# Optimization experiments

Measured on AMD Instinct MI355X. Metric: run time of the kernel, lower is better.

Reference implementation:

```python
import jax, jax.numpy as jnp
import numpy as np
import math

N_HEADS = 16
EMBED = 1024
D_KEY = EMBED // N_HEADS
B, S = 2, 2048
NEG = -1000000000.0


def setup_inputs() -> dict:
    key = jax.random.key(0)
    ks = jax.random.split(key, 7)
    scale = 1.0 / math.sqrt(EMBED)
    x = jax.random.normal(ks[0], (B, S, EMBED), dtype=jnp.float32)
    Wq_w = jax.random.uniform(ks[1], (EMBED, EMBED), jnp.float32, -scale, scale)
    Wq_b = jax.random.uniform(ks[2], (EMBED,), jnp.float32, -scale, scale)
    Wk_w = jax.random.uniform(ks[3], (EMBED, EMBED), jnp.float32, -scale, scale)
    Wk_b = jax.random.uniform(ks[4], (EMBED,), jnp.float32, -scale, scale)
    Wv_w = jax.random.uniform(ks[5], (EMBED, EMBED), jnp.float32, -scale, scale)
    Wv_b = jax.random.uniform(ks[6], (EMBED,), jnp.float32, -scale, scale)
    return {"x": x, "Wq_w": Wq_w, "Wq_b": Wq_b, "Wk_w": Wk_w, "Wk_b": Wk_b,
            "Wv_w": Wv_w, "Wv_b": Wv_b, "is_masked": 1}


def reference(x, Wq_w, Wq_b, Wk_w, Wk_b, Wv_w, Wv_b, is_masked):
    b, s, e = x.shape
    # nn.Linear: y = x @ W.T + b
    q = x @ Wq_w.T + Wq_b
    k = x @ Wk_w.T + Wk_b
    v = x @ Wv_w.T + Wv_b
    # [B, H, S, Dk]
    q = q.reshape(b, s, N_HEADS, D_KEY).transpose(0, 2, 1, 3)
    k = k.reshape(b, s, N_HEADS, D_KEY).transpose(0, 2, 1, 3)
    v = v.reshape(b, s, N_HEADS, D_KEY).transpose(0, 2, 1, 3)
    scores = jnp.einsum("bhqd,bhkd->bhqk", q, k) / math.sqrt(D_KEY)
    # non-standard mask: keep positions where score != padding (0)
    mask = scores != 0.0
    if is_masked:
        causal = jnp.tril(jnp.ones((1, s, s), dtype=bool))  # broadcasts over B,H
        mask = causal[None] & mask  # [1,1,S,S] & [B,H,S,S]
    scores = jnp.where(mask, scores, NEG)
    probs = jax.nn.softmax(scores, axis=-1)
    out = jnp.einsum("bhqk,bhkd->bhqd", probs, v)
    return out.transpose(0, 2, 1, 3).reshape(b, s, e)
```

## Files before the change

kernel.cpp:

```cpp
#include <hip/hip_runtime.h>

#define B_SZ   2
#define NH     16
#define S_LEN  2048
#define DK     64
#define EMB    1024
#define M_TOT  (B_SZ * S_LEN)
#define KT     64

typedef float          f32x4  __attribute__((ext_vector_type(4)));
typedef float          f32x16 __attribute__((ext_vector_type(16)));
typedef unsigned int   u32x4  __attribute__((ext_vector_type(4)));
typedef unsigned short u16x8  __attribute__((ext_vector_type(8)));
typedef unsigned short u16x4  __attribute__((ext_vector_type(4)));
typedef __bf16         bf16x8 __attribute__((ext_vector_type(8)));

static __device__ __forceinline__ f32x4 mfma16(u16x8 a, u16x8 b, f32x4 c) {
    return __builtin_amdgcn_mfma_f32_16x16x32_bf16(
        __builtin_bit_cast(bf16x8, a), __builtin_bit_cast(bf16x8, b), c, 0, 0, 0);
}
static __device__ __forceinline__ f32x16 mfma32(u16x8 a, u16x8 b, f32x16 c) {
    return __builtin_amdgcn_mfma_f32_32x32x16_bf16(
        __builtin_bit_cast(bf16x8, a), __builtin_bit_cast(bf16x8, b), c, 0, 0, 0);
}

static __device__ __forceinline__ unsigned short f2bf(float f) {
    unsigned int u = __builtin_bit_cast(unsigned int, f);
    u = (u + 0x7FFFu + ((u >> 16) & 1u)) >> 16;
    return (unsigned short)u;
}

static __device__ __forceinline__ float exp2_hw(float x) {
    float r; asm("v_exp_f32 %0, %1" : "=v"(r) : "v"(x)); return r;
}

#define GLDS16(g, l)  __builtin_amdgcn_global_load_lds(                      \
    (const void __attribute__((address_space(1)))*)(g),                      \
    (void __attribute__((address_space(3)))*)(l), 16, 0, 0)

__global__ __launch_bounds__(256) void cvt_kernel(
    const float* __restrict__ x,  const float* __restrict__ wq,
    const float* __restrict__ wk, const float* __restrict__ wv,
    unsigned short* __restrict__ xb,  unsigned short* __restrict__ wqb,
    unsigned short* __restrict__ wkb, unsigned short* __restrict__ wvb)
{
    long gid = (long)blockIdx.x * 256 + threadIdx.x;
    long e = gid * 4;
    const float* src; unsigned short* dst; long off;
    if      (e < 4194304L) { src = x;  dst = xb;  off = e; }
    else if (e < 5242880L) { src = wq; dst = wqb; off = e - 4194304L; }
    else if (e < 6291456L) { src = wk; dst = wkb; off = e - 5242880L; }
    else                   { src = wv; dst = wvb; off = e - 6291456L; }
    f32x4 v = *(const f32x4*)(src + off);
    u16x4 u;
    u[0] = f2bf(v[0]); u[1] = f2bf(v[1]); u[2] = f2bf(v[2]); u[3] = f2bf(v[3]);
    *(u16x4*)(dst + off) = u;
}

#define BM 128
#define BN 128
#define BK 64

__global__ __launch_bounds__(256) void qkv_gemm(
    const unsigned short* __restrict__ xb,
    const unsigned short* __restrict__ wb,
    const float* __restrict__ bq, const float* __restrict__ bk,
    const float* __restrict__ bv,
    unsigned short* __restrict__ qkv)
{
    const int tid  = threadIdx.x;
    const int lane = tid & 63;
    const int wid  = tid >> 6;
    const int wm   = wid >> 1, wn = wid & 1;
    const int n0   = blockIdx.x * BN;
    const int m0   = blockIdx.y * BM;
    const int mat  = blockIdx.z;

    const unsigned short* wmat = wb + (size_t)mat * (1024 * 1024);
    const float* bias = (mat == 0) ? bq : ((mat == 1) ? bk : bv);
    unsigned short* dst = qkv + (size_t)mat * ((size_t)M_TOT * EMB);

    __shared__ __align__(16) unsigned short Al[BM * 64];
    __shared__ __align__(16) unsigned short Bl[BN * 64];

    f32x4 acc[4][4];
#pragma unroll
    for (int i = 0; i < 4; ++i)
#pragma unroll
        for (int j = 0; j < 4; ++j)
            acc[i][j] = (f32x4){0.f, 0.f, 0.f, 0.f};

    const int wrow = wid * 32;
    const int lrow = lane >> 3;
    const int lcol = ((lane & 7) ^ lrow) * 8;
    const int l15  = lane & 15;
    const int sl0 = (((lane >> 4))     ^ (l15 & 7)) * 8;
    const int sl1 = ((4 + (lane >> 4)) ^ (l15 & 7)) * 8;

    for (int k0 = 0; k0 < EMB; k0 += BK) {
        const unsigned short* ga = xb   + (size_t)(m0 + wrow + lrow) * EMB + k0 + lcol;
        const unsigned short* gb = wmat + (size_t)(n0 + wrow + lrow) * EMB + k0 + lcol;
#pragma unroll
        for (int j = 0; j < 4; ++j) {
            GLDS16(ga + (size_t)j * 8 * EMB, &Al[(wrow + j * 8) * 64]);
            GLDS16(gb + (size_t)j * 8 * EMB, &Bl[(wrow + j * 8) * 64]);
        }
        __syncthreads();

#pragma unroll
        for (int kk = 0; kk < 2; ++kk) {
            const int sl = kk ? sl1 : sl0;
            u16x8 a[4], b[4];
#pragma unroll
            for (int i = 0; i < 4; ++i)
                a[i] = *(const u16x8*)&Al[(wm * 64 + i * 16 + l15) * 64 + sl];
#pragma unroll
            for (int j = 0; j < 4; ++j)
                b[j] = *(const u16x8*)&Bl[(wn * 64 + j * 16 + l15) * 64 + sl];
#pragma unroll
            for (int i = 0; i < 4; ++i)
#pragma unroll
                for (int j = 0; j < 4; ++j)
                    acc[i][j] = mfma16(a[i], b[j], acc[i][j]);
        }
        __syncthreads();
    }

#pragma unroll
    for (int j = 0; j < 4; ++j) {
        int n = n0 + wn * 64 + j * 16 + l15;
        float bvv = bias[n];
        int h = n >> 6, d = n & 63;
#pragma unroll
        for (int i = 0; i < 4; ++i) {
#pragma unroll
            for (int r = 0; r < 4; ++r) {
                int m = m0 + wm * 64 + i * 16 + ((lane >> 4) << 2) + r;
                int bb = m >> 11, s = m & 2047;
                dst[((size_t)((bb * NH + h) * S_LEN + s)) * DK + d] =
                    f2bf(acc[i][j][r] + bvv);
            }
        }
    }
}

__global__ __launch_bounds__(512) void attn_kernel(
    const unsigned short* __restrict__ Q,
    const unsigned short* __restrict__ K,
    const unsigned short* __restrict__ V,
    const int* __restrict__ mskp,
    float* __restrict__ out)
{
    const int tid = threadIdx.x, lane = tid & 63, wid = tid >> 6;
    const int grp = wid >> 2, qw = wid & 3;
    const int l31 = lane & 31, H = lane >> 5;
    const int bh = blockIdx.x;
    const int h  = bh & 15, b = bh >> 4;
    const int y  = blockIdx.y;
    const int qt = (y < 8) ? y : 23 - y;
    const int q0 = qt * 128;
    const size_t hoff = ((size_t)(b * NH + h)) * S_LEN * DK;
    const unsigned short* Qh = Q + hoff;
    const unsigned short* Kh = K + hoff;
    const unsigned short* Vh = V + hoff;
    const int msk = *mskp;
    const int ntiles = msk ? (2 * qt + 2) : (S_LEN / KT);
    const int niter  = ntiles >> 1;

    __shared__ __align__(16) unsigned short Kl[2][2][64 * 64];
    __shared__ __align__(16) unsigned short Vt[2][2][64 * 64];
    __shared__ float MLbuf[512];

    const int qrow = q0 + qw * 32 + l31;
    u16x8 qf[4];
#pragma unroll
    for (int ks = 0; ks < 4; ++ks)
        qf[ks] = *(const u16x8*)(Qh + (size_t)qrow * DK + ks * 16 + H * 8);

    u16x8 ones1;
#pragma unroll
    for (int i = 0; i < 8; ++i) ones1[i] = 0x3F80;

    f32x16 o0, o1, lacc;
#pragma unroll
    for (int i = 0; i < 16; ++i) { o0[i] = 0.f; o1[i] = 0.f; lacc[i] = 0.f; }
    float mx = -1e30f;

    const int gt  = tid & 255;
    const int sr0 = gt >> 3, sc8 = gt & 7, sr1 = sr0 + 32;
    const int kwo0 = sr0 * 64 + ((sc8 ^ (sr0 & 7)) << 3);
    const int kwo1 = sr1 * 64 + ((sc8 ^ (sr1 & 7)) << 3);
    const int vwo0 = (((sr0 >> 3) ^ sc8) << 3) + (sr0 & 7);
    const int vwo1 = (((sr1 >> 3) ^ sc8) << 3) + (sr1 & 7);

    const int qmin = q0 + qw * 32;
    const int dsw0 = l31 >> 3, dsw1 = 4 + (l31 >> 3);
    const int rsw  = l31 & 7;
    const float SC2 = 0.125f * 1.4426950408889634f;

    u16x8 kr[2], vr[2];
    {
        const unsigned short* K0 = Kh + (size_t)grp * KT * DK;
        const unsigned short* V0 = Vh + (size_t)grp * KT * DK;
        kr[0] = *(const u16x8*)(K0 + (size_t)sr0 * DK + sc8 * 8);
        vr[0] = *(const u16x8*)(V0 + (size_t)sr0 * DK + sc8 * 8);
        kr[1] = *(const u16x8*)(K0 + (size_t)sr1 * DK + sc8 * 8);
        vr[1] = *(const u16x8*)(V0 + (size_t)sr1 * DK + sc8 * 8);
        unsigned short* Kg = Kl[grp][0];
        unsigned short* Vg = Vt[grp][0];
        *(u16x8*)&Kg[kwo0] = kr[0];
        *(u16x8*)&Kg[kwo1] = kr[1];
#pragma unroll
        for (int e = 0; e < 8; ++e) {
            Vg[(sc8 * 8 + e) * 64 + vwo0] = vr[0][e];
            Vg[(sc8 * 8 + e) * 64 + vwo1] = vr[1][e];
        }
        if (grp + 2 < ntiles) {
            const unsigned short* Kn = Kh + (size_t)(grp + 2) * KT * DK;
            const unsigned short* Vn = Vh + (size_t)(grp + 2) * KT * DK;
            kr[0] = *(const u16x8*)(Kn + (size_t)sr0 * DK + sc8 * 8);
            vr[0] = *(const u16x8*)(Vn + (size_t)sr0 * DK + sc8 * 8);
            kr[1] = *(const u16x8*)(Kn + (size_t)sr1 * DK + sc8 * 8);
            vr[1] = *(const u16x8*)(Vn + (size_t)sr1 * DK + sc8 * 8);
        }
    }
    __syncthreads();

    int cur = 0;
    for (int it = 0; it < niter; ++it) {
        const int kt = 2 * it + grp;

        if (kt + 2 < ntiles) {
            unsigned short* Kg = Kl[grp][cur ^ 1];
            unsigned short* Vg = Vt[grp][cur ^ 1];
            *(u16x8*)&Kg[kwo0] = kr[0];
            *(u16x8*)&Kg[kwo1] = kr[1];
#pragma unroll
            for (int e = 0; e < 8; ++e) {
                Vg[(sc8 * 8 + e) * 64 + vwo0] = vr[0][e];
                Vg[(sc8 * 8 + e) * 64 + vwo1] = vr[1][e];
            }
        }
        if (kt + 4 < ntiles) {
            const unsigned short* Kn = Kh + (size_t)(kt + 4) * KT * DK;
            const unsigned short* Vn = Vh + (size_t)(kt + 4) * KT * DK;
            kr[0] = *(const u16x8*)(Kn + (size_t)sr0 * DK + sc8 * 8);
            vr[0] = *(const u16x8*)(Vn + (size_t)sr0 * DK + sc8 * 8);
            kr[1] = *(const u16x8*)(Kn + (size_t)sr1 * DK + sc8 * 8);
            vr[1] = *(const u16x8*)(Vn + (size_t)sr1 * DK + sc8 * 8);
        }

        if (!(msk && kt * KT > qmin + 31)) {
            const unsigned short* Kg = Kl[grp][cur];
            const unsigned short* Vg = Vt[grp][cur];

            f32x16 st0, st1;
#pragma unroll
            for (int i = 0; i < 16; ++i) { st0[i] = 0.f; st1[i] = 0.f; }
            __builtin_amdgcn_s_setprio(1);
#pragma unroll
            for (int ks = 0; ks < 4; ++ks) {
                const int g = (((ks << 1) + H) ^ rsw) << 3;
                u16x8 kf0 = *(const u16x8*)&Kg[l31 * 64 + g];
                u16x8 kf1 = *(const u16x8*)&Kg[(32 + l31) * 64 + g];
                st0 = mfma32(kf0, qf[ks], st0);
                st1 = mfma32(kf1, qf[ks], st1);
            }
            __builtin_amdgcn_s_setprio(0);

            st0 *= SC2;
            st1 *= SC2;
            float p[32];
#pragma unroll
            for (int r = 0; r < 16; ++r) { p[r] = st0[r]; p[16 + r] = st1[r]; }
            const bool needmask = msk && (kt * KT + 63 > qrow);
            if (needmask) {
#pragma unroll
                for (int r = 0; r < 16; ++r) {
                    const int krow = (r & 3) + 8 * (r >> 2) + 4 * H;
                    if (kt * KT + krow > qrow)      p[r]      = -1e30f;
                    if (kt * KT + 32 + krow > qrow) p[16 + r] = -1e30f;
                }
            }

            float t8[8];
#pragma unroll
            for (int i = 0; i < 8; ++i)
                t8[i] = fmaxf(fmaxf(p[i], p[i + 8]), fmaxf(p[i + 16], p[i + 24]));
#pragma unroll
            for (int i = 0; i < 4; ++i) t8[i] = fmaxf(t8[i], t8[i + 4]);
            float mt = fmaxf(fmaxf(t8[0], t8[1]), fmaxf(t8[2], t8[3]));
            mt = fmaxf(mt, __shfl_xor(mt, 32, 64));

            if (!__all(mt <= mx + 11.54f)) {
                const float mn = fmaxf(mx, mt);
                const float al = exp2_hw(mx - mn);
                mx = mn;
                o0 *= al; o1 *= al;
                lacc[0] *= al;
            }

#pragma unroll
            for (int r = 0; r < 32; ++r) p[r] = exp2_hw(p[r] - mx);

            __builtin_amdgcn_s_setprio(1);
#pragma unroll
            for (int ks = 0; ks < 4; ++ks) {
                const int bb = ks * 8;
                unsigned int wa, wb2, wc, wd;
                asm("v_cvt_pk_bf16_f32 %0, %1, %2" : "=v"(wa)  : "v"(p[bb + 0]), "v"(p[bb + 1]));
                asm("v_cvt_pk_bf16_f32 %0, %1, %2" : "=v"(wb2) : "v"(p[bb + 2]), "v"(p[bb + 3]));
                asm("v_cvt_pk_bf16_f32 %0, %1, %2" : "=v"(wc)  : "v"(p[bb + 4]), "v"(p[bb + 5]));
                asm("v_cvt_pk_bf16_f32 %0, %1, %2" : "=v"(wd)  : "v"(p[bb + 6]), "v"(p[bb + 7]));
                asm volatile("v_permlane32_swap_b32 %0, %1" : "+v"(wa),  "+v"(wc));
                asm volatile("v_permlane32_swap_b32 %0, %1" : "+v"(wb2), "+v"(wd));
                u32x4 wv; wv[0] = wa; wv[1] = wb2; wv[2] = wc; wv[3] = wd;
                const u16x8 pb = __builtin_bit_cast(u16x8, wv);
                const int kg = (ks << 1) + H;
                u16x8 vf0 = *(const u16x8*)&Vg[l31 * 64        + ((kg ^ dsw0) << 3)];
                u16x8 vf1 = *(const u16x8*)&Vg[(32 + l31) * 64 + ((kg ^ dsw1) << 3)];
                o0 = mfma32(vf0, pb, o0);
                o1 = mfma32(vf1, pb, o1);
                lacc = mfma32(ones1, pb, lacc);
            }
            __builtin_amdgcn_s_setprio(0);
        }

        __syncthreads();
        cur ^= 1;
    }

    const int idx = qw * 64 + lane;
    float* MO = (float*)Kl + idx * 32;
    const float lsum = lacc[0];
    if (grp == 1) {
#pragma unroll
        for (int i = 0; i < 16; ++i) {
            MO[(i + idx) & 31]      = o0[i];
            MO[(16 + i + idx) & 31] = o1[i];
        }
        MLbuf[idx * 2]     = mx;
        MLbuf[idx * 2 + 1] = lsum;
    }
    __syncthreads();
    if (grp == 0) {
        const float m2 = MLbuf[idx * 2], l2 = MLbuf[idx * 2 + 1];
        const float mn = fmaxf(mx, m2);
        const float ea = exp2_hw(mx - mn);
        const float eb = exp2_hw(m2 - mn);
        const float inv = 1.f / (lsum * ea + l2 * eb);
        float* orow = out + ((size_t)(b * S_LEN) + qrow) * EMB + h * DK;
#pragma unroll
        for (int g = 0; g < 4; ++g) {
            f32x4 w0, w1;
#pragma unroll
            for (int i = 0; i < 4; ++i) {
                w0[i] = (o0[4 * g + i] * ea + MO[(4 * g + i + idx) & 31] * eb) * inv;
                w1[i] = (o1[4 * g + i] * ea + MO[(16 + 4 * g + i + idx) & 31] * eb) * inv;
            }
            *(f32x4*)&orow[8 * g + 4 * H]      = w0;
            *(f32x4*)&orow[32 + 8 * g + 4 * H] = w1;
        }
    }
}

extern "C" void kernel_launch(void* const* d_in, const int* in_sizes, int n_in,
                              void* d_out, int out_size, void* d_ws, size_t ws_size,
                              hipStream_t stream)
{
    const float* x  = (const float*)d_in[0];
    const float* wq = (const float*)d_in[1];
    const float* bq = (const float*)d_in[2];
    const float* wk = (const float*)d_in[3];
    const float* bk = (const float*)d_in[4];
    const float* wv = (const float*)d_in[5];
    const float* bv = (const float*)d_in[6];
    const int* msk  = (const int*)d_in[7];
    float* out = (float*)d_out;

    unsigned short* xb  = (unsigned short*)d_ws;
    unsigned short* wb  = xb + (size_t)M_TOT * EMB;
    unsigned short* qkv = wb + (size_t)3 * 1024 * 1024;

    cvt_kernel<<<7168, 256, 0, stream>>>(x, wq, wk, wv,
                                         xb, wb, wb + 1024 * 1024, wb + 2 * 1024 * 1024);
    qkv_gemm<<<dim3(8, 32, 3), 256, 0, stream>>>(xb, wb, bq, bk, bv, qkv);
    attn_kernel<<<dim3(32, 16, 1), 512, 0, stream>>>(
        qkv, qkv + (size_t)M_TOT * EMB, qkv + (size_t)2 * M_TOT * EMB, msk, out);
}
```

Measured before the change: 91.77 us.

## Split KV across four wave groups and pair causal query tiles per block

The attention kernel now launches 1024-thread blocks with four KV-splitting wave groups instead of two. Each block handles two query tiles (qt and 15-qt) in sequence so causal work is balanced per block, and the grid is halved. Double buffering is dropped in favour of single-buffered shared tiles per group with two barriers per iteration. Partial results are merged through a two-level shared-memory reduction. This raises KV parallelism and balances the causal triangle, at the cost of extra synchronisation, lost load/compute overlap, and fewer blocks in flight.

```diff
diff --git a/kernel.cpp b/kernel.cpp
--- a/kernel.cpp
+++ b/kernel.cpp
@@ -144,7 +144,7 @@
     }
 }
 
-__global__ __launch_bounds__(512) void attn_kernel(
+__global__ __launch_bounds__(1024, 4) void attn_kernel(
     const unsigned short* __restrict__ Q,
     const unsigned short* __restrict__ K,
     const unsigned short* __restrict__ V,
@@ -156,35 +156,22 @@
     const int l31 = lane & 31, H = lane >> 5;
     const int bh = blockIdx.x;
     const int h  = bh & 15, b = bh >> 4;
-    const int y  = blockIdx.y;
-    const int qt = (y < 8) ? y : 23 - y;
-    const int q0 = qt * 128;
+    const int yp = blockIdx.y;
     const size_t hoff = ((size_t)(b * NH + h)) * S_LEN * DK;
     const unsigned short* Qh = Q + hoff;
     const unsigned short* Kh = K + hoff;
     const unsigned short* Vh = V + hoff;
     const int msk = *mskp;
-    const int ntiles = msk ? (2 * qt + 2) : (S_LEN / KT);
-    const int niter  = ntiles >> 1;
-
-    __shared__ __align__(16) unsigned short Kl[2][2][64 * 64];
-    __shared__ __align__(16) unsigned short Vt[2][2][64 * 64];
-    __shared__ float MLbuf[512];
-
-    const int qrow = q0 + qw * 32 + l31;
-    u16x8 qf[4];
-#pragma unroll
-    for (int ks = 0; ks < 4; ++ks)
-        qf[ks] = *(const u16x8*)(Qh + (size_t)qrow * DK + ks * 16 + H * 8);
+
+    __shared__ __align__(16) unsigned short Kl[4][64 * 64];
+    __shared__ __align__(16) unsigned short Vt[4][64 * 64];
+    __shared__ float MLbuf[3 * 512];
+    unsigned short* Kg = Kl[grp];
+    unsigned short* Vg = Vt[grp];
 
     u16x8 ones1;
 #pragma unroll
     for (int i = 0; i < 8; ++i) ones1[i] = 0x3F80;
-
-    f32x16 o0, o1, lacc;
-#pragma unroll
-    for (int i = 0; i < 16; ++i) { o0[i] = 0.f; o1[i] = 0.f; lacc[i] = 0.f; }
-    float mx = -1e30f;
 
     const int gt  = tid & 255;
     const int sr0 = gt >> 3, sc8 = gt & 7, sr1 = sr0 + 32;
@@ -193,21 +180,39 @@
     const int vwo0 = (((sr0 >> 3) ^ sc8) << 3) + (sr0 & 7);
     const int vwo1 = (((sr1 >> 3) ^ sc8) << 3) + (sr1 & 7);
 
-    const int qmin = q0 + qw * 32;
     const int dsw0 = l31 >> 3, dsw1 = 4 + (l31 >> 3);
     const int rsw  = l31 & 7;
     const float SC2 = 0.125f * 1.4426950408889634f;
-
-    u16x8 kr[2], vr[2];
-    {
-        const unsigned short* K0 = Kh + (size_t)grp * KT * DK;
-        const unsigned short* V0 = Vh + (size_t)grp * KT * DK;
-        kr[0] = *(const u16x8*)(K0 + (size_t)sr0 * DK + sc8 * 8);
-        vr[0] = *(const u16x8*)(V0 + (size_t)sr0 * DK + sc8 * 8);
-        kr[1] = *(const u16x8*)(K0 + (size_t)sr1 * DK + sc8 * 8);
-        vr[1] = *(const u16x8*)(V0 + (size_t)sr1 * DK + sc8 * 8);
-        unsigned short* Kg = Kl[grp][0];
-        unsigned short* Vg = Vt[grp][0];
+    const int idx  = qw * 64 + lane;
+
+    for (int seg = 0; seg < 2; ++seg) {
+        const int qt = seg ? (15 - yp) : yp;
+        const int q0 = qt * 128;
+        const int ntiles = msk ? (2 * qt + 2) : (S_LEN / KT);
+        const int niter  = (ntiles + 3) >> 2;
+        const int qrow = q0 + qw * 32 + l31;
+        const int qmin = q0 + qw * 32;
+
+        u16x8 qf[4];
+#pragma unroll
+        for (int ks = 0; ks < 4; ++ks)
+            qf[ks] = *(const u16x8*)(Qh + (size_t)qrow * DK + ks * 16 + H * 8);
+
+        f32x16 o0, o1, lacc;
+#pragma unroll
+        for (int i = 0; i < 16; ++i) { o0[i] = 0.f; o1[i] = 0.f; lacc[i] = 0.f; }
+        float mx = -1e30f;
+
+        u16x8 kr[2], vr[2];
+        {
+            const unsigned short* K0 = Kh + (size_t)grp * KT * DK;
+            const unsigned short* V0 = Vh + (size_t)grp * KT * DK;
+            kr[0] = *(const u16x8*)(K0 + (size_t)sr0 * DK + sc8 * 8);
+            vr[0] = *(const u16x8*)(V0 + (size_t)sr0 * DK + sc8 * 8);
+            kr[1] = *(const u16x8*)(K0 + (size_t)sr1 * DK + sc8 * 8);
+            vr[1] = *(const u16x8*)(V0 + (size_t)sr1 * DK + sc8 * 8);
+        }
+        __syncthreads();
         *(u16x8*)&Kg[kwo0] = kr[0];
         *(u16x8*)&Kg[kwo1] = kr[1];
 #pragma unroll
@@ -215,151 +220,176 @@
             Vg[(sc8 * 8 + e) * 64 + vwo0] = vr[0][e];
             Vg[(sc8 * 8 + e) * 64 + vwo1] = vr[1][e];
         }
-        if (grp + 2 < ntiles) {
-            const unsigned short* Kn = Kh + (size_t)(grp + 2) * KT * DK;
-            const unsigned short* Vn = Vh + (size_t)(grp + 2) * KT * DK;
+        if (grp + 4 < ntiles) {
+            const unsigned short* Kn = Kh + (size_t)(grp + 4) * KT * DK;
+            const unsigned short* Vn = Vh + (size_t)(grp + 4) * KT * DK;
             kr[0] = *(const u16x8*)(Kn + (size_t)sr0 * DK + sc8 * 8);
             vr[0] = *(const u16x8*)(Vn + (size_t)sr0 * DK + sc8 * 8);
             kr[1] = *(const u16x8*)(Kn + (size_t)sr1 * DK + sc8 * 8);
             vr[1] = *(const u16x8*)(Vn + (size_t)sr1 * DK + sc8 * 8);
         }
-    }
-    __syncthreads();
-
-    int cur = 0;
-    for (int it = 0; it < niter; ++it) {
-        const int kt = 2 * it + grp;
-
-        if (kt + 2 < ntiles) {
-            unsigned short* Kg = Kl[grp][cur ^ 1];
-            unsigned short* Vg = Vt[grp][cur ^ 1];
-            *(u16x8*)&Kg[kwo0] = kr[0];
-            *(u16x8*)&Kg[kwo1] = kr[1];
-#pragma unroll
-            for (int e = 0; e < 8; ++e) {
-                Vg[(sc8 * 8 + e) * 64 + vwo0] = vr[0][e];
-                Vg[(sc8 * 8 + e) * 64 + vwo1] = vr[1][e];
-            }
-        }
-        if (kt + 4 < ntiles) {
-            const unsigned short* Kn = Kh + (size_t)(kt + 4) * KT * DK;
-            const unsigned short* Vn = Vh + (size_t)(kt + 4) * KT * DK;
-            kr[0] = *(const u16x8*)(Kn + (size_t)sr0 * DK + sc8 * 8);
-            vr[0] = *(const u16x8*)(Vn + (size_t)sr0 * DK + sc8 * 8);
-            kr[1] = *(const u16x8*)(Kn + (size_t)sr1 * DK + sc8 * 8);
-            vr[1] = *(const u16x8*)(Vn + (size_t)sr1 * DK + sc8 * 8);
-        }
-
-        if (!(msk && kt * KT > qmin + 31)) {
-            const unsigned short* Kg = Kl[grp][cur];
-            const unsigned short* Vg = Vt[grp][cur];
-
-            f32x16 st0, st1;
-#pragma unroll
-            for (int i = 0; i < 16; ++i) { st0[i] = 0.f; st1[i] = 0.f; }
-            __builtin_amdgcn_s_setprio(1);
-#pragma unroll
-            for (int ks = 0; ks < 4; ++ks) {
-                const int g = (((ks << 1) + H) ^ rsw) << 3;
-                u16x8 kf0 = *(const u16x8*)&Kg[l31 * 64 + g];
-                u16x8 kf1 = *(const u16x8*)&Kg[(32 + l31) * 64 + g];
-                st0 = mfma32(kf0, qf[ks], st0);
-                st1 = mfma32(kf1, qf[ks], st1);
-            }
-            __builtin_amdgcn_s_setprio(0);
-
-            st0 *= SC2;
-            st1 *= SC2;
-            float p[32];
-#pragma unroll
-            for (int r = 0; r < 16; ++r) { p[r] = st0[r]; p[16 + r] = st1[r]; }
-            const bool needmask = msk && (kt * KT + 63 > qrow);
-            if (needmask) {
-#pragma unroll
-                for (int r = 0; r < 16; ++r) {
-                    const int krow = (r & 3) + 8 * (r >> 2) + 4 * H;
-                    if (kt * KT + krow > qrow)      p[r]      = -1e30f;
-                    if (kt * KT + 32 + krow > qrow) p[16 + r] = -1e30f;
-                }
-            }
-
-            float t8[8];
-#pragma unroll
-            for (int i = 0; i < 8; ++i)
-                t8[i] = fmaxf(fmaxf(p[i], p[i + 8]), fmaxf(p[i + 16], p[i + 24]));
-#pragma unroll
-            for (int i = 0; i < 4; ++i) t8[i] = fmaxf(t8[i], t8[i + 4]);
-            float mt = fmaxf(fmaxf(t8[0], t8[1]), fmaxf(t8[2], t8[3]));
-            mt = fmaxf(mt, __shfl_xor(mt, 32, 64));
-
-            if (!__all(mt <= mx + 11.54f)) {
-                const float mn = fmaxf(mx, mt);
-                const float al = exp2_hw(mx - mn);
-                mx = mn;
-                o0 *= al; o1 *= al;
-                lacc[0] *= al;
-            }
-
-#pragma unroll
-            for (int r = 0; r < 32; ++r) p[r] = exp2_hw(p[r] - mx);
-
-            __builtin_amdgcn_s_setprio(1);
-#pragma unroll
-            for (int ks = 0; ks < 4; ++ks) {
-                const int bb = ks * 8;
-                unsigned int wa, wb2, wc, wd;
-                asm("v_cvt_pk_bf16_f32 %0, %1, %2" : "=v"(wa)  : "v"(p[bb + 0]), "v"(p[bb + 1]));
-                asm("v_cvt_pk_bf16_f32 %0, %1, %2" : "=v"(wb2) : "v"(p[bb + 2]), "v"(p[bb + 3]));
-                asm("v_cvt_pk_bf16_f32 %0, %1, %2" : "=v"(wc)  : "v"(p[bb + 4]), "v"(p[bb + 5]));
-                asm("v_cvt_pk_bf16_f32 %0, %1, %2" : "=v"(wd)  : "v"(p[bb + 6]), "v"(p[bb + 7]));
-                asm volatile("v_permlane32_swap_b32 %0, %1" : "+v"(wa),  "+v"(wc));
-                asm volatile("v_permlane32_swap_b32 %0, %1" : "+v"(wb2), "+v"(wd));
-                u32x4 wv; wv[0] = wa; wv[1] = wb2; wv[2] = wc; wv[3] = wd;
-                const u16x8 pb = __builtin_bit_cast(u16x8, wv);
-                const int kg = (ks << 1) + H;
-                u16x8 vf0 = *(const u16x8*)&Vg[l31 * 64        + ((kg ^ dsw0) << 3)];
-                u16x8 vf1 = *(const u16x8*)&Vg[(32 + l31) * 64 + ((kg ^ dsw1) << 3)];
-                o0 = mfma32(vf0, pb, o0);
-                o1 = mfma32(vf1, pb, o1);
-                lacc = mfma32(ones1, pb, lacc);
-            }
-            __builtin_amdgcn_s_setprio(0);
-        }
-
-        __syncthreads();
-        cur ^= 1;
-    }
-
-    const int idx = qw * 64 + lane;
-    float* MO = (float*)Kl + idx * 32;
-    const float lsum = lacc[0];
-    if (grp == 1) {
-#pragma unroll
-        for (int i = 0; i < 16; ++i) {
-            MO[(i + idx) & 31]      = o0[i];
-            MO[(16 + i + idx) & 31] = o1[i];
-        }
-        MLbuf[idx * 2]     = mx;
-        MLbuf[idx * 2 + 1] = lsum;
-    }
-    __syncthreads();
-    if (grp == 0) {
-        const float m2 = MLbuf[idx * 2], l2 = MLbuf[idx * 2 + 1];
-        const float mn = fmaxf(mx, m2);
-        const float ea = exp2_hw(mx - mn);
-        const float eb = exp2_hw(m2 - mn);
-        const float inv = 1.f / (lsum * ea + l2 * eb);
-        float* orow = out + ((size_t)(b * S_LEN) + qrow) * EMB + h * DK;
-#pragma unroll
-        for (int g = 0; g < 4; ++g) {
-            f32x4 w0, w1;
-#pragma unroll
-            for (int i = 0; i < 4; ++i) {
-                w0[i] = (o0[4 * g + i] * ea + MO[(4 * g + i + idx) & 31] * eb) * inv;
-                w1[i] = (o1[4 * g + i] * ea + MO[(16 + 4 * g + i + idx) & 31] * eb) * inv;
-            }
-            *(f32x4*)&orow[8 * g + 4 * H]      = w0;
-            *(f32x4*)&orow[32 + 8 * g + 4 * H] = w1;
+        __syncthreads();
+
+        for (int it = 0; it < niter; ++it) {
+            const int kt = 4 * it + grp;
+
+            if (kt < ntiles && !(msk && kt * KT > qmin + 31)) {
+                f32x16 st0, st1;
+#pragma unroll
+                for (int i = 0; i < 16; ++i) { st0[i] = 0.f; st1[i] = 0.f; }
+                __builtin_amdgcn_s_setprio(1);
+#pragma unroll
+                for (int ks = 0; ks < 4; ++ks) {
+                    const int g = (((ks << 1) + H) ^ rsw) << 3;
+                    u16x8 kf0 = *(const u16x8*)&Kg[l31 * 64 + g];
+                    u16x8 kf1 = *(const u16x8*)&Kg[(32 + l31) * 64 + g];
+                    st0 = mfma32(kf0, qf[ks], st0);
+                    st1 = mfma32(kf1, qf[ks], st1);
+                }
+                __builtin_amdgcn_s_setprio(0);
+
+                st0 *= SC2;
+                st1 *= SC2;
+                float p[32];
+#pragma unroll
+                for (int r = 0; r < 16; ++r) { p[r] = st0[r]; p[16 + r] = st1[r]; }
+                const bool needmask = msk && (kt * KT + 63 > qrow);
+                if (needmask) {
+#pragma unroll
+                    for (int r = 0; r < 16; ++r) {
+                        const int krow = (r & 3) + 8 * (r >> 2) + 4 * H;
+                        if (kt * KT + krow > qrow)      p[r]      = -1e30f;
+                        if (kt * KT + 32 + krow > qrow) p[16 + r] = -1e30f;
+                    }
+                }
+
+                float t8[8];
+#pragma unroll
+                for (int i = 0; i < 8; ++i)
+                    t8[i] = fmaxf(fmaxf(p[i], p[i + 8]), fmaxf(p[i + 16], p[i + 24]));
+#pragma unroll
+                for (int i = 0; i < 4; ++i) t8[i] = fmaxf(t8[i], t8[i + 4]);
+                float mt = fmaxf(fmaxf(t8[0], t8[1]), fmaxf(t8[2], t8[3]));
+                mt = fmaxf(mt, __shfl_xor(mt, 32, 64));
+
+                if (!__all(mt <= mx + 11.54f)) {
+                    const float mn = fmaxf(mx, mt);
+                    const float al = exp2_hw(mx - mn);
+                    mx = mn;
+                    o0 *= al; o1 *= al;
+                    lacc[0] *= al;
+                }
+
+#pragma unroll
+                for (int r = 0; r < 32; ++r) p[r] = exp2_hw(p[r] - mx);
+
+                __builtin_amdgcn_s_setprio(1);
+#pragma unroll
+                for (int ks = 0; ks < 4; ++ks) {
+                    const int bb = ks * 8;
+                    unsigned int wa, wb2, wc, wd;
+                    asm("v_cvt_pk_bf16_f32 %0, %1, %2" : "=v"(wa)  : "v"(p[bb + 0]), "v"(p[bb + 1]));
+                    asm("v_cvt_pk_bf16_f32 %0, %1, %2" : "=v"(wb2) : "v"(p[bb + 2]), "v"(p[bb + 3]));
+                    asm("v_cvt_pk_bf16_f32 %0, %1, %2" : "=v"(wc)  : "v"(p[bb + 4]), "v"(p[bb + 5]));
+                    asm("v_cvt_pk_bf16_f32 %0, %1, %2" : "=v"(wd)  : "v"(p[bb + 6]), "v"(p[bb + 7]));
+                    asm volatile("v_permlane32_swap_b32 %0, %1" : "+v"(wa),  "+v"(wc));
+                    asm volatile("v_permlane32_swap_b32 %0, %1" : "+v"(wb2), "+v"(wd));
+                    u32x4 wv; wv[0] = wa; wv[1] = wb2; wv[2] = wc; wv[3] = wd;
+                    const u16x8 pb = __builtin_bit_cast(u16x8, wv);
+                    const int kg = (ks << 1) + H;
+                    u16x8 vf0 = *(const u16x8*)&Vg[l31 * 64        + ((kg ^ dsw0) << 3)];
+                    u16x8 vf1 = *(const u16x8*)&Vg[(32 + l31) * 64 + ((kg ^ dsw1) << 3)];
+                    o0 = mfma32(vf0, pb, o0);
+                    o1 = mfma32(vf1, pb, o1);
+                    lacc = mfma32(ones1, pb, lacc);
+                }
+                __builtin_amdgcn_s_setprio(0);
+            }
+
+            __syncthreads();
+            if (it + 1 < niter) {
+                const int ktn = 4 * (it + 1) + grp;
+                if (ktn < ntiles) {
+                    *(u16x8*)&Kg[kwo0] = kr[0];
+                    *(u16x8*)&Kg[kwo1] = kr[1];
+#pragma unroll
+                    for (int e = 0; e < 8; ++e) {
+                        Vg[(sc8 * 8 + e) * 64 + vwo0] = vr[0][e];
+                        Vg[(sc8 * 8 + e) * 64 + vwo1] = vr[1][e];
+                    }
+                }
+                if (ktn + 4 < ntiles) {
+                    const unsigned short* Kn = Kh + (size_t)(ktn + 4) * KT * DK;
+                    const unsigned short* Vn = Vh + (size_t)(ktn + 4) * KT * DK;
+                    kr[0] = *(const u16x8*)(Kn + (size_t)sr0 * DK + sc8 * 8);
+                    vr[0] = *(const u16x8*)(Vn + (size_t)sr0 * DK + sc8 * 8);
+                    kr[1] = *(const u16x8*)(Kn + (size_t)sr1 * DK + sc8 * 8);
+                    vr[1] = *(const u16x8*)(Vn + (size_t)sr1 * DK + sc8 * 8);
+                }
+                __syncthreads();
+            }
+        }
+
+        float lsum = lacc[0];
+        __syncthreads();
+        if (grp == 1 || grp == 3) {
+            float* MO = ((grp == 1) ? (float*)Kl : (float*)Vt) + idx * 32;
+#pragma unroll
+            for (int i = 0; i < 16; ++i) {
+                MO[(i + idx) & 31]      = o0[i];
+                MO[(16 + i + idx) & 31] = o1[i];
+            }
+            float* ML = MLbuf + (grp == 1 ? 0 : 512);
+            ML[idx * 2]     = mx;
+            ML[idx * 2 + 1] = lsum;
+        }
+        __syncthreads();
+        if (grp == 0 || grp == 2) {
+            const float* MO = ((grp == 0) ? (float*)Kl : (float*)Vt) + idx * 32;
+            const float* ML = MLbuf + (grp == 0 ? 0 : 512);
+            const float m2 = ML[idx * 2], l2 = ML[idx * 2 + 1];
+            const float mn = fmaxf(mx, m2);
+            const float ea = exp2_hw(mx - mn);
+            const float eb = exp2_hw(m2 - mn);
+            mx = mn;
+            lsum = lsum * ea + l2 * eb;
+#pragma unroll
+            for (int i = 0; i < 16; ++i) {
+                o0[i] = o0[i] * ea + MO[(i + idx) & 31] * eb;
+                o1[i] = o1[i] * ea + MO[(16 + i + idx) & 31] * eb;
+            }
+        }
+        __syncthreads();
+        if (grp == 2) {
+            float* MO = (float*)Kl + idx * 32;
+#pragma unroll
+            for (int i = 0; i < 16; ++i) {
+                MO[(i + idx) & 31]      = o0[i];
+                MO[(16 + i + idx) & 31] = o1[i];
+            }
+            MLbuf[1024 + idx * 2]     = mx;
+            MLbuf[1024 + idx * 2 + 1] = lsum;
+        }
+        __syncthreads();
+        if (grp == 0) {
+            const float* MO = (float*)Kl + idx * 32;
+            const float m2 = MLbuf[1024 + idx * 2], l2 = MLbuf[1024 + idx * 2 + 1];
+            const float mn = fmaxf(mx, m2);
+            const float ea = exp2_hw(mx - mn);
+            const float eb = exp2_hw(m2 - mn);
+            const float inv = 1.f / (lsum * ea + l2 * eb);
+            float* orow = out + ((size_t)(b * S_LEN) + qrow) * EMB + h * DK;
+#pragma unroll
+            for (int g = 0; g < 4; ++g) {
+                f32x4 w0, w1;
+#pragma unroll
+                for (int i = 0; i < 4; ++i) {
+                    w0[i] = (o0[4 * g + i] * ea + MO[(4 * g + i + idx) & 31] * eb) * inv;
+                    w1[i] = (o1[4 * g + i] * ea + MO[(16 + 4 * g + i + idx) & 31] * eb) * inv;
+                }
+                *(f32x4*)&orow[8 * g + 4 * H]      = w0;
+                *(f32x4*)&orow[32 + 8 * g + 4 * H] = w1;
+            }
         }
     }
 }
@@ -385,6 +415,6 @@
     cvt_kernel<<<7168, 256, 0, stream>>>(x, wq, wk, wv,
                                          xb, wb, wb + 1024 * 1024, wb + 2 * 1024 * 1024);
     qkv_gemm<<<dim3(8, 32, 3), 256, 0, stream>>>(xb, wb, bq, bk, bv, qkv);
-    attn_kernel<<<dim3(32, 16, 1), 512, 0, stream>>>(
+    attn_kernel<<<dim3(32, 8, 1), 1024, 0, stream>>>(
         qkv, qkv + (size_t)M_TOT * EMB, qkv + (size_t)2 * M_TOT * EMB, msk, out);
 }
```

Result: slower. 234.4 us (+155.5%).

## Rewrite QKV GEMM with 256x256 tiles and 4-stage async LDS pipeline

Applied to the files above, without the earlier changes.

Replaces the 128x128 single-buffered QKV projection GEMM with 256x256 tiles computed by 512 threads. K-slices of 32 are staged through a 4-deep ring of LDS buffers using global_load_lds. Manual vmcnt waits and raw barriers overlap the loads with MFMA work, and setprio is raised around the MFMA blocks. The three weight matrices are treated as one 3072-wide N dimension, which shrinks the grid to 192 blocks. The change targets load latency and sync stalls, at the cost of higher register and LDS pressure and fewer blocks in flight.

```diff
diff --git a/kernel.cpp b/kernel.cpp
--- a/kernel.cpp
+++ b/kernel.cpp
@@ -33,6 +33,13 @@
 static __device__ __forceinline__ float exp2_hw(float x) {
     float r; asm("v_exp_f32 %0, %1" : "=v"(r) : "v"(x)); return r;
 }
+
+static __device__ __forceinline__ void barrier_raw() {
+    asm volatile("s_barrier" ::: "memory");
+}
+#define VMCNT8() asm volatile("s_waitcnt vmcnt(8)" ::: "memory")
+#define VMCNT4() asm volatile("s_waitcnt vmcnt(4)" ::: "memory")
+#define VMCNT0() asm volatile("s_waitcnt vmcnt(0)" ::: "memory")
 
 #define GLDS16(g, l)  __builtin_amdgcn_global_load_lds(                      \
     (const void __attribute__((address_space(1)))*)(g),                      \
@@ -57,11 +64,7 @@
     *(u16x4*)(dst + off) = u;
 }
 
-#define BM 128
-#define BN 128
-#define BK 64
-
-__global__ __launch_bounds__(256) void qkv_gemm(
+__global__ __launch_bounds__(512) void qkv_gemm(
     const unsigned short* __restrict__ xb,
     const unsigned short* __restrict__ wb,
     const float* __restrict__ bq, const float* __restrict__ bk,
@@ -71,77 +74,112 @@
     const int tid  = threadIdx.x;
     const int lane = tid & 63;
     const int wid  = tid >> 6;
-    const int wm   = wid >> 1, wn = wid & 1;
-    const int n0   = blockIdx.x * BN;
-    const int m0   = blockIdx.y * BM;
-    const int mat  = blockIdx.z;
-
-    const unsigned short* wmat = wb + (size_t)mat * (1024 * 1024);
+    const int wm   = wid >> 2, wn = wid & 3;
+    const int n0   = blockIdx.x * 256;
+    const int m0   = blockIdx.y * 256;
+    const int l15  = lane & 15;
+    const int k4   = lane >> 4;
+
+    __shared__ __align__(16) unsigned short Al[4][256 * 32];
+    __shared__ __align__(16) unsigned short Bl[4][256 * 32];
+
+    f32x4 acc[8][4];
+#pragma unroll
+    for (int i = 0; i < 8; ++i)
+#pragma unroll
+        for (int j = 0; j < 4; ++j)
+            acc[i][j] = (f32x4){0.f, 0.f, 0.f, 0.f};
+
+    const int row0 = tid >> 2, row1 = (512 + tid) >> 2;
+    const int sl   = tid & 3;
+    const int c0   = (sl ^ (row0 & 3)) << 3;
+    const int c1   = (sl ^ (row1 & 3)) << 3;
+    const int d0   = (wid * 64) * 8;
+    const int d1   = (512 + wid * 64) * 8;
+    const unsigned short* gA0 = xb + (size_t)(m0 + row0) * EMB + c0;
+    const unsigned short* gA1 = xb + (size_t)(m0 + row1) * EMB + c1;
+    const unsigned short* gB0 = wb + (size_t)(n0 + row0) * EMB + c0;
+    const unsigned short* gB1 = wb + (size_t)(n0 + row1) * EMB + c1;
+
+#define STAGE_A(kt, b) do {                                     \
+        GLDS16(gA0 + (kt) * 32, &Al[b][d0]);                    \
+        GLDS16(gA1 + (kt) * 32, &Al[b][d1]); } while (0)
+#define STAGE_B(kt, b) do {                                     \
+        GLDS16(gB0 + (kt) * 32, &Bl[b][d0]);                    \
+        GLDS16(gB1 + (kt) * 32, &Bl[b][d1]); } while (0)
+
+    const int rsl = (k4 ^ (l15 & 3)) << 3;
+    const int abase = wm * 128 + l15;
+    const int bbase = wn * 64 + l15;
+
+    STAGE_A(0, 0); STAGE_B(0, 0);
+    STAGE_A(1, 1); STAGE_B(1, 1);
+    STAGE_A(2, 2); STAGE_B(2, 2);
+    VMCNT8();
+    barrier_raw();
+
+    for (int kt = 0; kt < 32; ++kt) {
+        const int b = kt & 3;
+        const unsigned short* Ab = Al[b];
+        const unsigned short* Bb = Bl[b];
+
+        u16x8 bfr[4], afr[4];
+#pragma unroll
+        for (int j = 0; j < 4; ++j)
+            bfr[j] = *(const u16x8*)&Bb[(bbase + j * 16) * 32 + rsl];
+#pragma unroll
+        for (int i = 0; i < 4; ++i)
+            afr[i] = *(const u16x8*)&Ab[(abase + i * 16) * 32 + rsl];
+        if (kt + 3 < 32) STAGE_A(kt + 3, (kt + 3) & 3);
+        __builtin_amdgcn_s_setprio(1);
+#pragma unroll
+        for (int i = 0; i < 4; ++i)
+#pragma unroll
+            for (int j = 0; j < 4; ++j)
+                acc[i][j] = mfma16(afr[i], bfr[j], acc[i][j]);
+        __builtin_amdgcn_s_setprio(0);
+        barrier_raw();
+
+#pragma unroll
+        for (int i = 0; i < 4; ++i)
+            afr[i] = *(const u16x8*)&Ab[(abase + (4 + i) * 16) * 32 + rsl];
+        if (kt + 3 < 32) STAGE_B(kt + 3, (kt + 3) & 3);
+        __builtin_amdgcn_s_setprio(1);
+#pragma unroll
+        for (int i = 0; i < 4; ++i)
+#pragma unroll
+            for (int j = 0; j < 4; ++j)
+                acc[4 + i][j] = mfma16(afr[i], bfr[j], acc[4 + i][j]);
+        __builtin_amdgcn_s_setprio(0);
+
+        if (kt == 29)      VMCNT4();
+        else if (kt == 30) VMCNT0();
+        else               VMCNT8();
+        barrier_raw();
+    }
+
+    const int mat = n0 >> 10;
     const float* bias = (mat == 0) ? bq : ((mat == 1) ? bk : bv);
     unsigned short* dst = qkv + (size_t)mat * ((size_t)M_TOT * EMB);
-
-    __shared__ __align__(16) unsigned short Al[BM * 64];
-    __shared__ __align__(16) unsigned short Bl[BN * 64];
-
-    f32x4 acc[4][4];
-#pragma unroll
-    for (int i = 0; i < 4; ++i)
-#pragma unroll
-        for (int j = 0; j < 4; ++j)
-            acc[i][j] = (f32x4){0.f, 0.f, 0.f, 0.f};
-
-    const int wrow = wid * 32;
-    const int lrow = lane >> 3;
-    const int lcol = ((lane & 7) ^ lrow) * 8;
-    const int l15  = lane & 15;
-    const int sl0 = (((lane >> 4))     ^ (l15 & 7)) * 8;
-    const int sl1 = ((4 + (lane >> 4)) ^ (l15 & 7)) * 8;
-
-    for (int k0 = 0; k0 < EMB; k0 += BK) {
-        const unsigned short* ga = xb   + (size_t)(m0 + wrow + lrow) * EMB + k0 + lcol;
-        const unsigned short* gb = wmat + (size_t)(n0 + wrow + lrow) * EMB + k0 + lcol;
-#pragma unroll
-        for (int j = 0; j < 4; ++j) {
-            GLDS16(ga + (size_t)j * 8 * EMB, &Al[(wrow + j * 8) * 64]);
-            GLDS16(gb + (size_t)j * 8 * EMB, &Bl[(wrow + j * 8) * 64]);
-        }
-        __syncthreads();
-
-#pragma unroll
-        for (int kk = 0; kk < 2; ++kk) {
-            const int sl = kk ? sl1 : sl0;
-            u16x8 a[4], b[4];
-#pragma unroll
-            for (int i = 0; i < 4; ++i)
-                a[i] = *(const u16x8*)&Al[(wm * 64 + i * 16 + l15) * 64 + sl];
-#pragma unroll
-            for (int j = 0; j < 4; ++j)
-                b[j] = *(const u16x8*)&Bl[(wn * 64 + j * 16 + l15) * 64 + sl];
-#pragma unroll
-            for (int i = 0; i < 4; ++i)
-#pragma unroll
-                for (int j = 0; j < 4; ++j)
-                    acc[i][j] = mfma16(a[i], b[j], acc[i][j]);
-        }
-        __syncthreads();
-    }
-
-#pragma unroll
-    for (int j = 0; j < 4; ++j) {
-        int n = n0 + wn * 64 + j * 16 + l15;
-        float bvv = bias[n];
-        int h = n >> 6, d = n & 63;
-#pragma unroll
-        for (int i = 0; i < 4; ++i) {
-#pragma unroll
-            for (int r = 0; r < 4; ++r) {
-                int m = m0 + wm * 64 + i * 16 + ((lane >> 4) << 2) + r;
-                int bb = m >> 11, s = m & 2047;
+    const int nb = (n0 & 1023) + wn * 64;
+#pragma unroll
+    for (int fc = 0; fc < 4; ++fc) {
+        const int nl = nb + fc * 16 + l15;
+        const float bvv = bias[nl];
+        const int h = nl >> 6, d = nl & 63;
+#pragma unroll
+        for (int fr = 0; fr < 8; ++fr) {
+#pragma unroll
+            for (int rr = 0; rr < 4; ++rr) {
+                const int m = m0 + wm * 128 + fr * 16 + k4 * 4 + rr;
+                const int bb = m >> 11, s = m & 2047;
                 dst[((size_t)((bb * NH + h) * S_LEN + s)) * DK + d] =
-                    f2bf(acc[i][j][r] + bvv);
-            }
-        }
-    }
+                    f2bf(acc[fr][fc][rr] + bvv);
+            }
+        }
+    }
+#undef STAGE_A
+#undef STAGE_B
 }
 
 __global__ __launch_bounds__(512) void attn_kernel(
@@ -384,7 +422,7 @@
 
     cvt_kernel<<<7168, 256, 0, stream>>>(x, wq, wk, wv,
                                          xb, wb, wb + 1024 * 1024, wb + 2 * 1024 * 1024);
-    qkv_gemm<<<dim3(8, 32, 3), 256, 0, stream>>>(xb, wb, bq, bk, bv, qkv);
+    qkv_gemm<<<dim3(12, 16, 1), 512, 0, stream>>>(xb, wb, bq, bk, bv, qkv);
     attn_kernel<<<dim3(32, 16, 1), 512, 0, stream>>>(
         qkv, qkv + (size_t)M_TOT * EMB, qkv + (size_t)2 * M_TOT * EMB, msk, out);
 }
```

New measurement: 88.63 us. 1.04x faster.
